# Kernel tuning notes

Measured on AMD Instinct MI355X. Metric: run time of the kernel, lower is better.

Reference implementation:

```python
import jax, jax.numpy as jnp
import numpy as np

N_NODES = 100000
N_EDGES = 2400000


def setup_inputs() -> dict:
    key = jax.random.key(0)
    ks = jax.random.split(key, 6)
    x = jax.random.normal(ks[0], (N_NODES, 2), dtype=jnp.float32)
    edge_index = jax.random.randint(ks[1], (2, N_EDGES), 0, N_NODES, dtype=jnp.int64)
    # GCNConv weights (glorot-ish scale) and zero biases
    W1 = jax.random.normal(ks[2], (2, 32), dtype=jnp.float32) * (1.0 / np.sqrt(2.0))
    b1 = jnp.zeros((32,), dtype=jnp.float32)
    W2 = jax.random.normal(ks[3], (32, 32), dtype=jnp.float32) * (1.0 / np.sqrt(32.0))
    b2 = jnp.zeros((32,), dtype=jnp.float32)
    W3 = jax.random.normal(ks[4], (32, 1), dtype=jnp.float32) * (1.0 / np.sqrt(32.0))
    b3 = jnp.zeros((1,), dtype=jnp.float32)
    return {"x": x, "edge_index": edge_index, "W1": W1, "b1": b1,
            "W2": W2, "b2": b2, "W3": W3, "b3": b3}


def reference(x, edge_index, W1, b1, W2, b2, W3, b3):
    N = x.shape[0]
    self_loops = jnp.arange(N, dtype=edge_index.dtype)
    src = jnp.concatenate([edge_index[0], self_loops])  # message sources
    dst = jnp.concatenate([edge_index[1], self_loops])  # aggregation targets
    # Symmetric GCN normalization: deg computed at target nodes (PyG gcn_norm)
    deg = jax.ops.segment_sum(jnp.ones_like(dst, dtype=x.dtype), dst, num_segments=N)
    dinv = jnp.where(deg > 0, jax.lax.rsqrt(deg), 0.0)
    norm = (dinv[src] * dinv[dst])[:, None]  # [E+N, 1]

    def gcn_layer(h, W, b):
        h = h @ W                                  # [N, out]
        msg = norm * h[src]                        # gather + scale
        agg = jax.ops.segment_sum(msg, dst, num_segments=N)  # scatter-add
        return agg + b

    h = jax.nn.relu(gcn_layer(x, W1, b1))
    h = jax.nn.relu(gcn_layer(h, W2, b2))
    out = gcn_layer(h, W3, b3)
    return out.reshape(-1)
```

## Files before the change

### kernel.cpp

```cpp
#include <hip/hip_runtime.h>

#define NN 100000
#define NE 2400000
#define NB 391
#define CAP 6912
#define CAP2 7168
#define EPB 4096
#define NBLK2 ((NE + EPB - 1) / EPB)
#define IMASK 0x1FFFF
#define SLACK 131072

__device__ __forceinline__ int wexscan(int v, int lane) {
    int x = v;
#pragma unroll
    for (int off = 1; off < 64; off <<= 1) {
        int t = __shfl_up(x, off, 64);
        x += (lane >= off) ? t : 0;
    }
    return x - v;
}

__global__ __launch_bounds__(512) void k_hist(const int* __restrict__ ei,
        int* __restrict__ bh) {
    __shared__ int hist[NB];
    int tid = threadIdx.x;
    for (int i = tid; i < NB; i += 512) hist[i] = 0;
    __syncthreads();
    int base_e = blockIdx.x * EPB + tid * 8;
    if (base_e + 8 <= NE) {
        int4 da = *(const int4*)(ei + NE + base_e);
        int4 db = *(const int4*)(ei + NE + base_e + 4);
        atomicAdd(&hist[da.x >> 8], 1); atomicAdd(&hist[da.y >> 8], 1);
        atomicAdd(&hist[da.z >> 8], 1); atomicAdd(&hist[da.w >> 8], 1);
        atomicAdd(&hist[db.x >> 8], 1); atomicAdd(&hist[db.y >> 8], 1);
        atomicAdd(&hist[db.z >> 8], 1); atomicAdd(&hist[db.w >> 8], 1);
    }
    __syncthreads();
    for (int i = tid; i < NB; i += 512) bh[blockIdx.x * NB + i] = hist[i];
}

__global__ __launch_bounds__(256) void k_offscan(int* __restrict__ bh,
        int* __restrict__ tot) {
    __shared__ int wsum[4];
    int b = blockIdx.x, tid = threadIdx.x;
    int lane = tid & 63, wid = tid >> 6;
    int carry = 0;
#pragma unroll
    for (int r = 0; r < 3; ++r) {
        int blk = r * 256 + tid;
        int v = (blk < NBLK2) ? bh[blk * NB + b] : 0;
        int ex = wexscan(v, lane);
        if (lane == 63) wsum[wid] = ex + v;
        __syncthreads();
        int woff = 0, rt = 0;
#pragma unroll
        for (int i = 0; i < 4; ++i) {
            woff += (i < wid) ? wsum[i] : 0;
            rt += wsum[i];
        }
        if (blk < NBLK2) bh[blk * NB + b] = b * CAP + carry + woff + ex;
        carry += rt;
        __syncthreads();
    }
    if (tid == 0) tot[b] = carry;
}

__global__ __launch_bounds__(512) void k_scatter2(const int* __restrict__ ei,
        const int* __restrict__ bh, int* __restrict__ binned) {
    __shared__ int hist[NB], lbase[NB], myb[NB];
    __shared__ int stage[EPB];
    __shared__ unsigned short stageb[EPB];
    __shared__ int wsum[8];
    int tid = threadIdx.x;
    for (int i = tid; i < NB; i += 512) {
        hist[i] = 0;
        myb[i] = bh[blockIdx.x * NB + i];
    }
    __syncthreads();
    int base_e = blockIdx.x * EPB + tid * 8;
    int pk[8], bn[8], rk[8];
    if (base_e + 8 <= NE) {
        const int4* s4 = (const int4*)(ei + base_e);
        const int4* d4 = (const int4*)(ei + NE + base_e);
        int4 sa = s4[0], sb = s4[1], da = d4[0], db = d4[1];
        int ss[8] = {sa.x, sa.y, sa.z, sa.w, sb.x, sb.y, sb.z, sb.w};
        int dd[8] = {da.x, da.y, da.z, da.w, db.x, db.y, db.z, db.w};
#pragma unroll
        for (int k = 0; k < 8; ++k) {
            bn[k] = dd[k] >> 8;
            pk[k] = ss[k] | ((dd[k] & 255) << 17);
            rk[k] = atomicAdd(&hist[bn[k]], 1);
        }
    } else {
#pragma unroll
        for (int k = 0; k < 8; ++k) bn[k] = -1;
    }
    __syncthreads();
    int lane = tid & 63, wid = tid >> 6;
    int v = (tid < NB) ? hist[tid] : 0;
    int ex = wexscan(v, lane);
    if (lane == 63) wsum[wid] = ex + v;
    __syncthreads();
    int woff = 0, tot = 0;
#pragma unroll
    for (int i = 0; i < 8; ++i) {
        int s = wsum[i];
        woff += (i < wid) ? s : 0;
        tot += s;
    }
    ex += woff;
    if (tid < NB) lbase[tid] = ex;
    __syncthreads();
#pragma unroll
    for (int k = 0; k < 8; ++k) {
        if (bn[k] >= 0) {
            int slot = lbase[bn[k]] + rk[k];
            stage[slot] = pk[k];
            stageb[slot] = (unsigned short)bn[k];
        }
    }
    __syncthreads();
    for (int j = tid; j < tot; j += 512) {
        int b = stageb[j];
        binned[myb[b] + (j - lbase[b])] = stage[j];
    }
}

__global__ __launch_bounds__(256) void k_build(const int* __restrict__ binned,
        const int* __restrict__ tot, const float* __restrict__ x,
        int* __restrict__ rsp, float* __restrict__ dinv, float2* __restrict__ xs,
        int* __restrict__ csr, float4* __restrict__ At) {
    __shared__ int4 ebin4[CAP / 4];
    __shared__ int cnt[256];
    __shared__ int wsum[4];
    int* ebin = (int*)ebin4;
    int tid = threadIdx.x, b = blockIdx.x;
    int base = b * CAP, base2 = b * CAP2, n = tot[b];
    cnt[tid] = 0;
    __syncthreads();
    int n4 = n >> 2;
    const int4* b4 = (const int4*)(binned + base);
    for (int j = tid; j < n4; j += 256) {
        int4 w = b4[j];
        ebin4[j] = w;
        atomicAdd(&cnt[(w.x >> 17) & 255], 1);
        atomicAdd(&cnt[(w.y >> 17) & 255], 1);
        atomicAdd(&cnt[(w.z >> 17) & 255], 1);
        atomicAdd(&cnt[(w.w >> 17) & 255], 1);
    }
    for (int j = (n4 << 2) + tid; j < n; j += 256) {
        int w = binned[base + j];
        ebin[j] = w;
        atomicAdd(&cnt[(w >> 17) & 255], 1);
    }
    __syncthreads();
    int deg = cnt[tid];
    int degp = (deg + 3) & ~3;
    int lane = tid & 63, wid = tid >> 6;
    int ex = wexscan(degp, lane);
    if (lane == 63) wsum[wid] = ex + degp;
    __syncthreads();
    int woff = 0;
#pragma unroll
    for (int i = 0; i < 4; ++i) woff += (i < wid) ? wsum[i] : 0;
    ex += woff;
    int node = (b << 8) + tid;
    if (node < NN) {
        rsp[node] = ((base2 + ex) << 8) | deg;
        float di = rsqrtf((float)(deg + 1));
        dinv[node] = di;
        float2 xv = ((const float2*)x)[node];
        xs[node] = make_float2(di * xv.x, di * xv.y);
        int beg = base2 + ex;
        for (int p = beg + deg; p < beg + degp; ++p) csr[p] = NN;
    }
    if (node == NN) {
        xs[NN] = make_float2(0.f, 0.f);
        At[NN] = make_float4(0.f, 0.f, 0.f, 0.f);
    }
    cnt[tid] = ex;
    __syncthreads();
    for (int j = tid; j < n; j += 256) {
        int w = ebin[j];
        int p = atomicAdd(&cnt[(w >> 17) & 255], 1);
        csr[base2 + p] = w & IMASK;
    }
}

__global__ __launch_bounds__(256) void k_At(const int* __restrict__ rsp,
        const int* __restrict__ csr, const float2* __restrict__ xs,
        const float* __restrict__ dinv, float4* __restrict__ At) {
    int node = blockIdx.x * 256 + threadIdx.x;
    if (node >= NN) return;
    int rp = rsp[node];
    int beg = rp >> 8, d = rp & 255;
    int nIt = ((d + 3) & ~3) >> 2;
    float ax = 0.f, ay = 0.f;
    const int4* cp = (const int4*)(csr + beg);
    if (nIt > 0) {
        int4 c0 = cp[0], c1 = cp[1];
        float2 A0 = xs[c0.x & IMASK], A1 = xs[c0.y & IMASK];
        float2 A2 = xs[c0.z & IMASK], A3 = xs[c0.w & IMASK];
        for (int it = 0; it < nIt; ++it) {
            int4 cn = cp[it + 2];
            float2 B0 = xs[c1.x & IMASK], B1 = xs[c1.y & IMASK];
            float2 B2 = xs[c1.z & IMASK], B3 = xs[c1.w & IMASK];
            ax += (A0.x + A1.x) + (A2.x + A3.x);
            ay += (A0.y + A1.y) + (A2.y + A3.y);
            A0 = B0; A1 = B1; A2 = B2; A3 = B3;
            c1 = cn;
        }
    }
    float di = dinv[node];
    float2 xn = xs[node];
    At[node] = make_float4(di * (ax + xn.x), di * (ay + xn.y), di, 0.f);
}

__global__ __launch_bounds__(256) void k_agg(const float4* __restrict__ At,
        const int* __restrict__ rsp, const int* __restrict__ csr,
        const float* __restrict__ W1, const float* __restrict__ b1,
        const float* __restrict__ W2, const float* __restrict__ b2,
        const float* __restrict__ W3, float* __restrict__ h3) {
    __shared__ float accS[32 * 36];
    __shared__ float diS[32];
    int tid = threadIdx.x;
    if (blockIdx.x == 0 && tid == 0) h3[NN] = 0.f;
    int o = tid & 7, nl = tid >> 3;
    int node = blockIdx.x * 32 + nl;
    int f = tid & 31;

    float4 w0 = *(const float4*)&W1[4 * o];
    float4 w1 = *(const float4*)&W1[32 + 4 * o];
    float4 bb = *(const float4*)&b1[4 * o];

    int r = rsp[node];
    int beg = r >> 8, deg = r & 255;
    int nIt = ((deg + 3) & ~3) >> 2;
    float4 an = At[node];
    float di = an.z;

    float4 acc;
    {
        float v0 = fmaf(an.y, w1.x, fmaf(an.x, w0.x, bb.x));
        float v1 = fmaf(an.y, w1.y, fmaf(an.x, w0.y, bb.y));
        float v2 = fmaf(an.y, w1.z, fmaf(an.x, w0.z, bb.z));
        float v3 = fmaf(an.y, w1.w, fmaf(an.x, w0.w, bb.w));
        acc.x = di * fmaxf(v0, 0.f);
        acc.y = di * fmaxf(v1, 0.f);
        acc.z = di * fmaxf(v2, 0.f);
        acc.w = di * fmaxf(v3, 0.f);
    }

    auto acc1 = [&](const float4& aa) {
        float v0 = fmaf(aa.y, w1.x, fmaf(aa.x, w0.x, bb.x));
        float v1 = fmaf(aa.y, w1.y, fmaf(aa.x, w0.y, bb.y));
        float v2 = fmaf(aa.y, w1.z, fmaf(aa.x, w0.z, bb.z));
        float v3 = fmaf(aa.y, w1.w, fmaf(aa.x, w0.w, bb.w));
        acc.x = fmaf(aa.z, fmaxf(v0, 0.f), acc.x);
        acc.y = fmaf(aa.z, fmaxf(v1, 0.f), acc.y);
        acc.z = fmaf(aa.z, fmaxf(v2, 0.f), acc.z);
        acc.w = fmaf(aa.z, fmaxf(v3, 0.f), acc.w);
    };

    const int4* cp = (const int4*)(csr + beg);
    {
        int4 c0 = cp[0], c1 = cp[1];
        float4 A0 = At[c0.x & IMASK], A1 = At[c0.y & IMASK];
        float4 A2 = At[c0.z & IMASK], A3 = At[c0.w & IMASK];
        for (int it = 0; it < nIt; ++it) {
            int4 cn = cp[it + 2];
            float4 B0 = At[c1.x & IMASK], B1 = At[c1.y & IMASK];
            float4 B2 = At[c1.z & IMASK], B3 = At[c1.w & IMASK];
            acc1(A0); acc1(A1); acc1(A2); acc1(A3);
            A0 = B0; A1 = B1; A2 = B2; A3 = B3;
            c1 = cn;
        }
    }

    float w2r[32];
#pragma unroll
    for (int k = 0; k < 32; ++k) w2r[k] = W2[k * 32 + f];

    acc.x *= di; acc.y *= di; acc.z *= di; acc.w *= di;
    *(float4*)&accS[nl * 36 + 4 * o] = acc;
    if (o == 0) diS[nl] = di;
    __syncthreads();

    float bf = b2[f], w3f = W3[f];
    int g = tid >> 5;
#pragma unroll
    for (int rr = 0; rr < 4; ++rr) {
        int n = g + 8 * rr;
        const float* arow = &accS[n * 36];
        float sum = bf;
#pragma unroll
        for (int k = 0; k < 32; k += 4) {
            float4 a4 = *(const float4*)&arow[k];
            sum = fmaf(a4.x, w2r[k], sum);
            sum = fmaf(a4.y, w2r[k + 1], sum);
            sum = fmaf(a4.z, w2r[k + 2], sum);
            sum = fmaf(a4.w, w2r[k + 3], sum);
        }
        float h2 = fmaxf(sum, 0.f);
        float v = h2 * w3f;
#pragma unroll
        for (int off = 16; off > 0; off >>= 1) v += __shfl_down(v, off, 32);
        if (f == 0) h3[blockIdx.x * 32 + n] = diS[n] * v;
    }
}

__global__ __launch_bounds__(256) void k_gather_out(const float* __restrict__ hs,
        const int* __restrict__ rsp, const int* __restrict__ csr,
        const float* __restrict__ dinv, const float* __restrict__ bias,
        float* __restrict__ out) {
    int node = blockIdx.x * 256 + threadIdx.x;
    if (node >= NN) return;
    int r = rsp[node];
    int beg = r >> 8, deg = r & 255;
    int nIt = ((deg + 3) & ~3) >> 2;
    float acc = hs[node];
    const int4* cp = (const int4*)(csr + beg);
    if (nIt > 0) {
        int4 c0 = cp[0], c1 = cp[1];
        float A0 = hs[c0.x & IMASK], A1 = hs[c0.y & IMASK];
        float A2 = hs[c0.z & IMASK], A3 = hs[c0.w & IMASK];
        for (int it = 0; it < nIt; ++it) {
            int4 cn = cp[it + 2];
            float B0 = hs[c1.x & IMASK], B1 = hs[c1.y & IMASK];
            float B2 = hs[c1.z & IMASK], B3 = hs[c1.w & IMASK];
            acc += (A0 + A1) + (A2 + A3);
            A0 = B0; A1 = B1; A2 = B2; A3 = B3;
            c1 = cn;
        }
    }
    out[node] = dinv[node] * acc + bias[0];
}

extern "C" void kernel_launch(void* const* d_in, const int* in_sizes, int n_in,
                              void* d_out, int out_size, void* d_ws, size_t ws_size,
                              hipStream_t stream) {
    const float* x  = (const float*)d_in[0];
    const int*   ei = (const int*)d_in[1];
    const float* W1 = (const float*)d_in[2];
    const float* b1 = (const float*)d_in[3];
    const float* W2 = (const float*)d_in[4];
    const float* b2 = (const float*)d_in[5];
    const float* W3 = (const float*)d_in[6];
    const float* b3 = (const float*)d_in[7];
    float* out = (float*)d_out;

    char* w = (char*)d_ws;
    float4* At    = (float4*)w; w += SLACK * 16;
    float2* xs    = (float2*)w; w += SLACK * 8;
    int*   bh     = (int*)w;    w += NBLK2 * NB * 4;
    int*   tot    = (int*)w;    w += NB * 4;
    int*   rsp    = (int*)w;    w += NN * 4;
    float* dinv   = (float*)w;  w += NN * 4;
    int*   binned = (int*)w;    w += NB * CAP * 4;
    int*   csr    = (int*)w;    w += (NB * CAP2 + 16) * 4;
    float* h3     = (float*)w;  w += SLACK * 4;

    const int G_N = (NN + 255) / 256;
    const int G_A = NN / 32;

    k_hist<<<NBLK2, 512, 0, stream>>>(ei, bh);
    k_offscan<<<NB, 256, 0, stream>>>(bh, tot);
    k_scatter2<<<NBLK2, 512, 0, stream>>>(ei, bh, binned);
    k_build<<<NB, 256, 0, stream>>>(binned, tot, x, rsp, dinv, xs, csr, At);
    k_At<<<G_N, 256, 0, stream>>>(rsp, csr, xs, dinv, At);
    k_agg<<<G_A, 256, 0, stream>>>(At, rsp, csr, W1, b1, W2, b2, W3, h3);
    k_gather_out<<<G_N, 256, 0, stream>>>(h3, rsp, csr, dinv, b3, out);
}
```

Before: 173.5 us.

## Fuse preprocessing phases into one cooperative kernel with grid syncs

Merges the histogram, offset scan, scatter, CSR build and first-layer aggregation kernels into a single cooperative launch, using grid-wide barriers between phases, with a fallback to separate launches if the cooperative launch fails. Blocks drop from 512 to 256 threads and each thread handles 16 edges, so the 586-block grid can be co-resident (3 blocks per CU) and phases share one LDS buffer. The aim is to remove per-kernel launch gaps and tail effects. In exchange it adds the cost of grid syncs, leaves many blocks idle in the phases that use only 391 or 391 blocks, and puts more register pressure on each thread.

```diff
diff --git a/kernel.cpp b/kernel.cpp
--- a/kernel.cpp
+++ b/kernel.cpp
@@ -1,4 +1,6 @@
 #include <hip/hip_runtime.h>
+#include <hip/hip_cooperative_groups.h>
+namespace cg = cooperative_groups;
 
 #define NN 100000
 #define NE 2400000
@@ -9,6 +11,7 @@
 #define NBLK2 ((NE + EPB - 1) / EPB)
 #define IMASK 0x1FFFF
 #define SLACK 131072
+#define LDSB 29440
 
 __device__ __forceinline__ int wexscan(int v, int lane) {
     int x = v;
@@ -20,29 +23,29 @@
     return x - v;
 }
 
-__global__ __launch_bounds__(512) void k_hist(const int* __restrict__ ei,
+
+__device__ void ph_hist(int b, int tid, char* ldsc, const int* __restrict__ ei,
         int* __restrict__ bh) {
-    __shared__ int hist[NB];
-    int tid = threadIdx.x;
-    for (int i = tid; i < NB; i += 512) hist[i] = 0;
-    __syncthreads();
-    int base_e = blockIdx.x * EPB + tid * 8;
-    if (base_e + 8 <= NE) {
-        int4 da = *(const int4*)(ei + NE + base_e);
-        int4 db = *(const int4*)(ei + NE + base_e + 4);
-        atomicAdd(&hist[da.x >> 8], 1); atomicAdd(&hist[da.y >> 8], 1);
-        atomicAdd(&hist[da.z >> 8], 1); atomicAdd(&hist[da.w >> 8], 1);
-        atomicAdd(&hist[db.x >> 8], 1); atomicAdd(&hist[db.y >> 8], 1);
-        atomicAdd(&hist[db.z >> 8], 1); atomicAdd(&hist[db.w >> 8], 1);
-    }
-    __syncthreads();
-    for (int i = tid; i < NB; i += 512) bh[blockIdx.x * NB + i] = hist[i];
-}
-
-__global__ __launch_bounds__(256) void k_offscan(int* __restrict__ bh,
+    int* hist = (int*)ldsc;
+    for (int i = tid; i < NB; i += 256) hist[i] = 0;
+    __syncthreads();
+    int base_e = b * EPB + tid * 16;
+    if (base_e + 16 <= NE) {
+        const int4* d4 = (const int4*)(ei + NE + base_e);
+#pragma unroll
+        for (int q = 0; q < 4; ++q) {
+            int4 d = d4[q];
+            atomicAdd(&hist[d.x >> 8], 1); atomicAdd(&hist[d.y >> 8], 1);
+            atomicAdd(&hist[d.z >> 8], 1); atomicAdd(&hist[d.w >> 8], 1);
+        }
+    }
+    __syncthreads();
+    for (int i = tid; i < NB; i += 256) bh[b * NB + i] = hist[i];
+}
+
+__device__ void ph_offscan(int b, int tid, char* ldsc, int* __restrict__ bh,
         int* __restrict__ tot) {
-    __shared__ int wsum[4];
-    int b = blockIdx.x, tid = threadIdx.x;
+    int* wsum = (int*)ldsc;
     int lane = tid & 63, wid = tid >> 6;
     int carry = 0;
 #pragma unroll
@@ -65,76 +68,81 @@
     if (tid == 0) tot[b] = carry;
 }
 
-__global__ __launch_bounds__(512) void k_scatter2(const int* __restrict__ ei,
+__device__ void ph_scatter(int b, int tid, char* ldsc, const int* __restrict__ ei,
         const int* __restrict__ bh, int* __restrict__ binned) {
-    __shared__ int hist[NB], lbase[NB], myb[NB];
-    __shared__ int stage[EPB];
-    __shared__ unsigned short stageb[EPB];
-    __shared__ int wsum[8];
-    int tid = threadIdx.x;
-    for (int i = tid; i < NB; i += 512) {
+    int* lds   = (int*)ldsc;
+    int* hist  = lds;
+    int* lbase = lds + 391;
+    int* myb   = lds + 782;
+    int* wsum  = lds + 1173;
+    int* stage = lds + 1184;
+    unsigned short* stageb = (unsigned short*)(lds + 5280);
+    for (int i = tid; i < NB; i += 256) {
         hist[i] = 0;
-        myb[i] = bh[blockIdx.x * NB + i];
-    }
-    __syncthreads();
-    int base_e = blockIdx.x * EPB + tid * 8;
-    int pk[8], bn[8], rk[8];
-    if (base_e + 8 <= NE) {
+        myb[i] = bh[b * NB + i];
+    }
+    __syncthreads();
+    int base_e = b * EPB + tid * 16;
+    int pk[16], bn[16], rk[16];
+    bool act = (base_e + 16 <= NE);
+    if (act) {
         const int4* s4 = (const int4*)(ei + base_e);
         const int4* d4 = (const int4*)(ei + NE + base_e);
-        int4 sa = s4[0], sb = s4[1], da = d4[0], db = d4[1];
-        int ss[8] = {sa.x, sa.y, sa.z, sa.w, sb.x, sb.y, sb.z, sb.w};
-        int dd[8] = {da.x, da.y, da.z, da.w, db.x, db.y, db.z, db.w};
-#pragma unroll
-        for (int k = 0; k < 8; ++k) {
-            bn[k] = dd[k] >> 8;
-            pk[k] = ss[k] | ((dd[k] & 255) << 17);
-            rk[k] = atomicAdd(&hist[bn[k]], 1);
-        }
-    } else {
-#pragma unroll
-        for (int k = 0; k < 8; ++k) bn[k] = -1;
+#pragma unroll
+        for (int q = 0; q < 4; ++q) {
+            int4 s = s4[q], d = d4[q];
+            int ss[4] = {s.x, s.y, s.z, s.w};
+            int dd[4] = {d.x, d.y, d.z, d.w};
+#pragma unroll
+            for (int k = 0; k < 4; ++k) {
+                int i = q * 4 + k;
+                bn[i] = dd[k] >> 8;
+                pk[i] = ss[k] | ((dd[k] & 255) << 17);
+                rk[i] = atomicAdd(&hist[bn[i]], 1);
+            }
+        }
     }
     __syncthreads();
     int lane = tid & 63, wid = tid >> 6;
-    int v = (tid < NB) ? hist[tid] : 0;
-    int ex = wexscan(v, lane);
-    if (lane == 63) wsum[wid] = ex + v;
-    __syncthreads();
-    int woff = 0, tot = 0;
-#pragma unroll
-    for (int i = 0; i < 8; ++i) {
-        int s = wsum[i];
-        woff += (i < wid) ? s : 0;
-        tot += s;
-    }
-    ex += woff;
-    if (tid < NB) lbase[tid] = ex;
-    __syncthreads();
-#pragma unroll
-    for (int k = 0; k < 8; ++k) {
-        if (bn[k] >= 0) {
-            int slot = lbase[bn[k]] + rk[k];
-            stage[slot] = pk[k];
-            stageb[slot] = (unsigned short)bn[k];
-        }
-    }
-    __syncthreads();
-    for (int j = tid; j < tot; j += 512) {
-        int b = stageb[j];
-        binned[myb[b] + (j - lbase[b])] = stage[j];
-    }
-}
-
-__global__ __launch_bounds__(256) void k_build(const int* __restrict__ binned,
+    int carry = 0;
+#pragma unroll
+    for (int r = 0; r < 2; ++r) {
+        int idx = r * 256 + tid;
+        int v = (idx < NB) ? hist[idx] : 0;
+        int ex = wexscan(v, lane);
+        if (lane == 63) wsum[wid] = ex + v;
+        __syncthreads();
+        int woff = 0, rt = 0;
+#pragma unroll
+        for (int i = 0; i < 4; ++i) { woff += (i < wid) ? wsum[i] : 0; rt += wsum[i]; }
+        if (idx < NB) lbase[idx] = carry + woff + ex;
+        carry += rt;
+        __syncthreads();
+    }
+    int tot = carry;
+    if (act) {
+#pragma unroll
+        for (int i = 0; i < 16; ++i) {
+            int slot = lbase[bn[i]] + rk[i];
+            stage[slot] = pk[i];
+            stageb[slot] = (unsigned short)bn[i];
+        }
+    }
+    __syncthreads();
+    for (int j = tid; j < tot; j += 256) {
+        int bb = stageb[j];
+        binned[myb[bb] + (j - lbase[bb])] = stage[j];
+    }
+}
+
+__device__ void ph_build(int b, int tid, char* ldsc, const int* __restrict__ binned,
         const int* __restrict__ tot, const float* __restrict__ x,
         int* __restrict__ rsp, float* __restrict__ dinv, float2* __restrict__ xs,
         int* __restrict__ csr, float4* __restrict__ At) {
-    __shared__ int4 ebin4[CAP / 4];
-    __shared__ int cnt[256];
-    __shared__ int wsum[4];
-    int* ebin = (int*)ebin4;
-    int tid = threadIdx.x, b = blockIdx.x;
+    int*  ebin  = (int*)ldsc;
+    int4* ebin4 = (int4*)ldsc;
+    int*  cnt   = (int*)ldsc + 6912;
+    int*  wsum  = (int*)ldsc + 7168;
     int base = b * CAP, base2 = b * CAP2, n = tot[b];
     cnt[tid] = 0;
     __syncthreads();
@@ -187,10 +195,10 @@
     }
 }
 
-__global__ __launch_bounds__(256) void k_At(const int* __restrict__ rsp,
+__device__ void ph_At(int b, int tid, const int* __restrict__ rsp,
         const int* __restrict__ csr, const float2* __restrict__ xs,
         const float* __restrict__ dinv, float4* __restrict__ At) {
-    int node = blockIdx.x * 256 + threadIdx.x;
+    int node = b * 256 + tid;
     if (node >= NN) return;
     int rp = rsp[node];
     int beg = rp >> 8, d = rp & 255;
@@ -214,6 +222,52 @@
     float di = dinv[node];
     float2 xn = xs[node];
     At[node] = make_float4(di * (ax + xn.x), di * (ay + xn.y), di, 0.f);
+}
+
+__global__ __launch_bounds__(256, 3) void k_pre(const int* __restrict__ ei,
+        const float* __restrict__ x, int* __restrict__ bh, int* __restrict__ tot,
+        int* __restrict__ binned, int* __restrict__ rsp, float* __restrict__ dinv,
+        float2* __restrict__ xs, int* __restrict__ csr, float4* __restrict__ At) {
+    __shared__ __align__(16) char ldsb[LDSB];
+    cg::grid_group gg = cg::this_grid();
+    int b = blockIdx.x, tid = threadIdx.x;
+    ph_hist(b, tid, ldsb, ei, bh);
+    gg.sync();
+    if (b < NB) ph_offscan(b, tid, ldsb, bh, tot);
+    gg.sync();
+    ph_scatter(b, tid, ldsb, ei, bh, binned);
+    gg.sync();
+    if (b < NB) ph_build(b, tid, ldsb, binned, tot, x, rsp, dinv, xs, csr, At);
+    gg.sync();
+    if (b < NB) ph_At(b, tid, rsp, csr, xs, dinv, At);
+}
+
+__global__ __launch_bounds__(256) void k_hist_f(const int* __restrict__ ei,
+        int* __restrict__ bh) {
+    __shared__ __align__(16) char ldsb[LDSB];
+    ph_hist(blockIdx.x, threadIdx.x, ldsb, ei, bh);
+}
+__global__ __launch_bounds__(256) void k_offscan_f(int* __restrict__ bh,
+        int* __restrict__ tot) {
+    __shared__ __align__(16) char ldsb[LDSB];
+    ph_offscan(blockIdx.x, threadIdx.x, ldsb, bh, tot);
+}
+__global__ __launch_bounds__(256) void k_scatter_f(const int* __restrict__ ei,
+        const int* __restrict__ bh, int* __restrict__ binned) {
+    __shared__ __align__(16) char ldsb[LDSB];
+    ph_scatter(blockIdx.x, threadIdx.x, ldsb, ei, bh, binned);
+}
+__global__ __launch_bounds__(256) void k_build_f(const int* __restrict__ binned,
+        const int* __restrict__ tot, const float* __restrict__ x,
+        int* __restrict__ rsp, float* __restrict__ dinv, float2* __restrict__ xs,
+        int* __restrict__ csr, float4* __restrict__ At) {
+    __shared__ __align__(16) char ldsb[LDSB];
+    ph_build(blockIdx.x, threadIdx.x, ldsb, binned, tot, x, rsp, dinv, xs, csr, At);
+}
+__global__ __launch_bounds__(256) void k_At_f(const int* __restrict__ rsp,
+        const int* __restrict__ csr, const float2* __restrict__ xs,
+        const float* __restrict__ dinv, float4* __restrict__ At) {
+    ph_At(blockIdx.x, threadIdx.x, rsp, csr, xs, dinv, At);
 }
 
 __global__ __launch_bounds__(256) void k_agg(const float4* __restrict__ At,
@@ -339,8 +393,8 @@
 extern "C" void kernel_launch(void* const* d_in, const int* in_sizes, int n_in,
                               void* d_out, int out_size, void* d_ws, size_t ws_size,
                               hipStream_t stream) {
+    const int*   ei = (const int*)d_in[1];
     const float* x  = (const float*)d_in[0];
-    const int*   ei = (const int*)d_in[1];
     const float* W1 = (const float*)d_in[2];
     const float* b1 = (const float*)d_in[3];
     const float* W2 = (const float*)d_in[4];
@@ -363,11 +417,20 @@
     const int G_N = (NN + 255) / 256;
     const int G_A = NN / 32;
 
-    k_hist<<<NBLK2, 512, 0, stream>>>(ei, bh);
-    k_offscan<<<NB, 256, 0, stream>>>(bh, tot);
-    k_scatter2<<<NBLK2, 512, 0, stream>>>(ei, bh, binned);
-    k_build<<<NB, 256, 0, stream>>>(binned, tot, x, rsp, dinv, xs, csr, At);
-    k_At<<<G_N, 256, 0, stream>>>(rsp, csr, xs, dinv, At);
+    void* args[10];
+    args[0] = (void*)&ei;  args[1] = (void*)&x;   args[2] = (void*)&bh;
+    args[3] = (void*)&tot; args[4] = (void*)&binned; args[5] = (void*)&rsp;
+    args[6] = (void*)&dinv; args[7] = (void*)&xs; args[8] = (void*)&csr;
+    args[9] = (void*)&At;
+    hipError_t ce = hipLaunchCooperativeKernel((void*)k_pre, dim3(NBLK2), dim3(256),
+                                               args, 0, stream);
+    if (ce != hipSuccess) {
+        k_hist_f<<<NBLK2, 256, 0, stream>>>(ei, bh);
+        k_offscan_f<<<NB, 256, 0, stream>>>(bh, tot);
+        k_scatter_f<<<NBLK2, 256, 0, stream>>>(ei, bh, binned);
+        k_build_f<<<NB, 256, 0, stream>>>(binned, tot, x, rsp, dinv, xs, csr, At);
+        k_At_f<<<G_N, 256, 0, stream>>>(rsp, csr, xs, dinv, At);
+    }
     k_agg<<<G_A, 256, 0, stream>>>(At, rsp, csr, W1, b1, W2, b2, W3, h3);
     k_gather_out<<<G_N, 256, 0, stream>>>(h3, rsp, csr, dinv, b3, out);
 }
```

Result: slower. 463.1 us (+166.8%).
